# Optimization experiments

Measured on AMD Instinct MI355X. Metric: run time of the kernel, lower is better.

The kernel has to match this reference:

```python
import jax, jax.numpy as jnp
import numpy as np

NUM_HEADS = 8
TAU = 2.0
BN_EPS = 1e-5


def _make_atan_spike(alpha):
    @jax.custom_vjp
    def spike(x):
        return (x >= 0.0).astype(x.dtype)
    def fwd(x):
        return spike(x), x
    def bwd(x, g):
        sg = (alpha / 2.0) / (1.0 + (jnp.pi / 2.0 * alpha * x) ** 2)
        return (g * sg,)
    spike.defvjp(fwd, bwd)
    return spike


def _make_sigmoid_spike(alpha):
    @jax.custom_vjp
    def spike(x):
        return (x >= 0.0).astype(x.dtype)
    def fwd(x):
        return spike(x), x
    def bwd(x, g):
        s = jax.nn.sigmoid(alpha * x)
        return (g * alpha * s * (1.0 - s),)
    spike.defvjp(fwd, bwd)
    return spike

_atan_spike = _make_atan_spike(5.0)       # surrogate.ATan(alpha=5.0)
_sigmoid_spike = _make_sigmoid_spike(4.0)  # spikingjelly default surrogate.Sigmoid(alpha=4.0)


def lif_multistep(x_seq, v_threshold, spike_fn):
    """Multi-step LIF, tau=2, hard reset to 0, detach_reset=True, decay_input=True.
    x_seq: [T, ...]. Returns spike sequence [T, ...]."""
    def step(v, x):
        h = v + (x - v) / TAU
        s = spike_fn(h - v_threshold)
        sd = jax.lax.stop_gradient(s)  # detach_reset
        v_new = h * (1.0 - sd)         # hard reset to v_reset=0
        return v_new, s
    _, s_seq = jax.lax.scan(step, jnp.zeros_like(x_seq[0]), x_seq)
    return s_seq


def bn(x, gamma, beta, mean, var):
    # inference-mode BatchNorm1d over channel dim C of [T,B,C,N]
    inv = gamma / jnp.sqrt(var + BN_EPS)
    return (x - mean[None, None, :, None]) * inv[None, None, :, None] + beta[None, None, :, None]


def setup_inputs() -> dict:
    key = jax.random.key(0)
    T, B, C, H, W = 4, 32, 384, 16, 16
    ks = jax.random.split(key, 20)
    d = {"x": jax.random.normal(ks[0], (T, B, C, H, W), dtype=jnp.float32)}
    std = 1.0 / np.sqrt(C)
    for i, p in enumerate(["q", "k", "proj"]):
        d[p + "_w"] = jax.random.normal(ks[1 + 5 * i], (C, C), dtype=jnp.float32) * std
        d[p + "_gamma"] = jnp.ones((C,), jnp.float32) + 0.1 * jax.random.normal(ks[2 + 5 * i], (C,))
        d[p + "_beta"] = 0.1 * jax.random.normal(ks[3 + 5 * i], (C,))
        d[p + "_mean"] = 0.1 * jax.random.normal(ks[4 + 5 * i], (C,))
        d[p + "_var"] = jax.random.uniform(ks[5 + 5 * i], (C,), minval=0.5, maxval=1.5)
    d["proj_b"] = 0.01 * jax.random.normal(ks[16], (C,))
    return d


def reference(x, q_w, q_gamma, q_beta, q_mean, q_var,
              k_w, k_gamma, k_beta, k_mean, k_var,
              proj_w, proj_gamma, proj_beta, proj_mean, proj_var, proj_b):
    T, B, C, H, W = x.shape
    N = H * W
    Ch = C // NUM_HEADS
    xf = x.reshape(T, B, C, N)

    # q branch: 1x1 conv (C x C matmul) -> BN -> LIF
    q = bn(jnp.einsum('tbcn,dc->tbdn', xf, q_w), q_gamma, q_beta, q_mean, q_var)
    q = lif_multistep(q, 1.0, _atan_spike)
    q = q.reshape(T, B, NUM_HEADS, Ch, N)
    q = jnp.sum(q, axis=3, keepdims=True)          # [T,B,h,1,N]
    attn = lif_multistep(q, 0.5, _sigmoid_spike)    # attn_lif, v_threshold=0.5

    # k branch
    k = bn(jnp.einsum('tbcn,dc->tbdn', xf, k_w), k_gamma, k_beta, k_mean, k_var)
    k = lif_multistep(k, 1.0, _atan_spike)
    k = k.reshape(T, B, NUM_HEADS, Ch, N)

    y = (attn * k).reshape(T, B, C, N)

    # proj: 1x1 conv with bias -> BN -> LIF
    y = jnp.einsum('tbcn,dc->tbdn', y, proj_w) + proj_b[None, None, :, None]
    y = bn(y, proj_gamma, proj_beta, proj_mean, proj_var)
    y = lif_multistep(y, 1.0, _atan_spike)
    return y.reshape(T, B, C, H, W)
```

## Files before the change

kernel.cpp:

```cpp
#include <hip/hip_runtime.h>

typedef _Float16 f16x8 __attribute__((ext_vector_type(8)));
typedef _Float16 f16x4 __attribute__((ext_vector_type(4)));
typedef float    f32x4 __attribute__((ext_vector_type(4)));

#define TT 4
#define BB 32
#define CC 384
#define NN 256

#define WS_X1   25165824
#define WS_WSP  50331648
#define WS_Y    52101120
#define WS_NEED 77266944

__global__ __launch_bounds__(256) void wprep(
    const float* __restrict__ qw, const float* __restrict__ kw,
    const float* __restrict__ pw, _Float16* __restrict__ wsp)
{
    int gid   = blockIdx.x * 256 + threadIdx.x;
    int which = gid / 18432;
    int sid   = gid % 18432;
    int frag  = sid >> 6;
    int lane  = sid & 63;
    int h  = frag / 36;
    int rm = frag % 36;
    int dt = rm / 12, kc = rm % 12;
    int m16 = lane & 15, quad = lane >> 4;
    int d = h * 48 + dt * 16 + m16;

    const float* src = (which == 0) ? qw : (which == 1) ? kw : pw;
    _Float16* o0 = wsp + (size_t)which * 294912;
    _Float16* o1 = o0 + 147456;

    f16x8 h0, h1;
#pragma unroll
    for (int j = 0; j < 8; ++j) {
        int cp = kc * 32 + quad * 8 + j;
        int c;
        if (which == 2) {
            int hp = cp / 48, w = cp % 48;
            int qp = w / 12, r12 = w % 12;
            int sl = r12 >> 2, rr = r12 & 3;
            c = hp * 48 + sl * 16 + qp * 4 + rr;
        } else {
            c = cp;
        }
        float v = src[d * CC + c];
        _Float16 a = (_Float16)v;
        h0[j] = a; h1[j] = (_Float16)(v - (float)a);
    }
    size_t off = (size_t)frag * 512 + lane * 8;
    *(f16x8*)(o0 + off) = h0;
    *(f16x8*)(o1 + off) = h1;
}

__global__ __launch_bounds__(256) void xprep(
    const float* __restrict__ x, _Float16* __restrict__ x0,
    _Float16* __restrict__ x1)
{
    __shared__ float xs[64 * 65];
    const int tid = threadIdx.x;
    int bid = blockIdx.x;
    int tb = bid / 24, r = bid % 24;
    int c0 = (r >> 2) * 64, n0 = (r & 3) * 64;

#pragma unroll
    for (int p = 0; p < 4; ++p) {
        int c  = (tid >> 4) + p * 16;
        int nl = (tid & 15) * 4;
        float4 v = *(const float4*)&x[((size_t)tb * CC + c0 + c) * NN + n0 + nl];
        *(float4*)&xs[c * 65 + nl] = v;
    }
    __syncthreads();
#pragma unroll
    for (int p = 0; p < 2; ++p) {
        int sid  = p * 256 + tid;
        int frag = sid >> 6;
        int lane = sid & 63;
        int kcl  = frag & 1, n16l = frag >> 1;
        int m16 = lane & 15, quad = lane >> 4;
        int n_local = n16l * 16 + m16;
        int c_local = kcl * 32 + quad * 8;
        f16x8 h0, h1;
#pragma unroll
        for (int j = 0; j < 8; ++j) {
            float v = xs[(c_local + j) * 65 + n_local];
            _Float16 a = (_Float16)v;
            h0[j] = a; h1[j] = (_Float16)(v - (float)a);
        }
        size_t gf = ((size_t)tb * 16 + (n0 >> 4) + n16l) * 12 + (c0 >> 5) + kcl;
        size_t off = gf * 512 + lane * 8;
        *(f16x8*)(x0 + off) = h0;
        *(f16x8*)(x1 + off) = h1;
    }
}

__global__ __launch_bounds__(256, 3) void qk_mfma(
    const _Float16* __restrict__ x0, const _Float16* __restrict__ x1,
    const _Float16* __restrict__ wsp,
    const float* __restrict__ qg, const float* __restrict__ qbe,
    const float* __restrict__ qm, const float* __restrict__ qva,
    const float* __restrict__ kg, const float* __restrict__ kbe,
    const float* __restrict__ km, const float* __restrict__ kva,
    _Float16* __restrict__ y)
{
    const int tid  = threadIdx.x;
    const int wave = tid >> 6;
    const int lane = tid & 63;
    const int m16  = lane & 15;
    const int quad = lane >> 4;

    int bid = blockIdx.x;
    int r   = bid & 7;
    int hh  = (bid >> 3) & 1;
    int qq  = bid >> 4;
    int j   = qq * 8 + r;
    int b   = j >> 4;
    int n16 = j & 15;

    const int head = hh * 4 + wave;

    const _Float16* wq0 = wsp;
    const _Float16* wq1 = wsp + 147456;
    const _Float16* wk0 = wsp + 2 * 147456;
    const _Float16* wk1 = wsp + 3 * 147456;

    size_t fxb[4];
#pragma unroll
    for (int t = 0; t < 4; ++t)
        fxb[t] = (((size_t)(t * BB + b) * 16 + n16) * 12) * 512 + lane * 8;
    size_t fwb = ((size_t)head * 36) * 512 + lane * 8;

    f32x4 aq[4][3], ak[4][3];
#pragma unroll
    for (int t = 0; t < 4; ++t)
#pragma unroll
        for (int dt = 0; dt < 3; ++dt) {
            aq[t][dt] = (f32x4){0.f, 0.f, 0.f, 0.f};
            ak[t][dt] = (f32x4){0.f, 0.f, 0.f, 0.f};
        }

    for (int kc = 0; kc < 12; ++kc) {
        f16x8 bx[4][2];
#pragma unroll
        for (int t = 0; t < 4; ++t) {
            bx[t][0] = *(const f16x8*)(x0 + fxb[t] + kc * 512);
            bx[t][1] = *(const f16x8*)(x1 + fxb[t] + kc * 512);
        }
#pragma unroll
        for (int dt = 0; dt < 3; ++dt) {
            size_t wo = fwb + (size_t)(dt * 12 + kc) * 512;
            f16x8 q0 = *(const f16x8*)(wq0 + wo);
            f16x8 q1 = *(const f16x8*)(wq1 + wo);
            f16x8 k0 = *(const f16x8*)(wk0 + wo);
            f16x8 k1 = *(const f16x8*)(wk1 + wo);
#pragma unroll
            for (int t = 0; t < 4; ++t) {
                f32x4 cq = aq[t][dt];
                cq = __builtin_amdgcn_mfma_f32_16x16x32_f16(q0, bx[t][0], cq, 0, 0, 0);
                cq = __builtin_amdgcn_mfma_f32_16x16x32_f16(q1, bx[t][0], cq, 0, 0, 0);
                cq = __builtin_amdgcn_mfma_f32_16x16x32_f16(q0, bx[t][1], cq, 0, 0, 0);
                aq[t][dt] = cq;
                f32x4 ck = ak[t][dt];
                ck = __builtin_amdgcn_mfma_f32_16x16x32_f16(k0, bx[t][0], ck, 0, 0, 0);
                ck = __builtin_amdgcn_mfma_f32_16x16x32_f16(k1, bx[t][0], ck, 0, 0, 0);
                ck = __builtin_amdgcn_mfma_f32_16x16x32_f16(k0, bx[t][1], ck, 0, 0, 0);
                ak[t][dt] = ck;
            }
        }
    }

    f32x4 vq[3], vk[3];
    float va = 0.f;
#pragma unroll
    for (int dt = 0; dt < 3; ++dt) {
        vq[dt] = (f32x4){0.f, 0.f, 0.f, 0.f};
        vk[dt] = (f32x4){0.f, 0.f, 0.f, 0.f};
    }
#pragma unroll
    for (int t = 0; t < 4; ++t) {
        float psum = 0.f;
        f32x4 ks[3];
#pragma unroll
        for (int dt = 0; dt < 3; ++dt) {
            int doff = head * 48 + dt * 16 + quad * 4;
            f32x4 gq  = *(const f32x4*)(qg + doff);
            f32x4 bq  = *(const f32x4*)(qbe + doff);
            f32x4 mq  = *(const f32x4*)(qm + doff);
            f32x4 vq_ = *(const f32x4*)(qva + doff);
            f32x4 gk_ = *(const f32x4*)(kg + doff);
            f32x4 bk_ = *(const f32x4*)(kbe + doff);
            f32x4 mk_ = *(const f32x4*)(km + doff);
            f32x4 vk_ = *(const f32x4*)(kva + doff);
#pragma unroll
            for (int rr = 0; rr < 4; ++rr) {
                float invq = gq[rr] / sqrtf(vq_[rr] + 1e-5f);
                float invk = gk_[rr] / sqrtf(vk_[rr] + 1e-5f);
                float bnq = (aq[t][dt][rr] - mq[rr]) * invq + bq[rr];
                float hq  = vq[dt][rr] + (bnq - vq[dt][rr]) * 0.5f;
                float sq  = (hq - 1.0f >= 0.0f) ? 1.0f : 0.0f;
                vq[dt][rr] = hq * (1.0f - sq);
                psum += sq;
                float bnk = (ak[t][dt][rr] - mk_[rr]) * invk + bk_[rr];
                float hk  = vk[dt][rr] + (bnk - vk[dt][rr]) * 0.5f;
                float sk  = (hk - 1.0f >= 0.0f) ? 1.0f : 0.0f;
                vk[dt][rr] = hk * (1.0f - sk);
                ks[dt][rr] = sk;
            }
        }
        psum += __shfl_xor(psum, 16, 64);
        psum += __shfl_xor(psum, 32, 64);
        float ha = va + (psum - va) * 0.5f;
        float sa = (ha - 0.5f >= 0.0f) ? 1.0f : 0.0f;
        va = ha * (1.0f - sa);
        float attn = sa;
        size_t ybase = (((size_t)(t * BB + b) * 16 + n16) * 12) * 512;
#pragma unroll
        for (int dt = 0; dt < 3; ++dt) {
            int c   = head * 48 + quad * 12 + dt * 4;
            int kcy = c >> 5;
            int qp  = (c & 31) >> 3;
            int jj  = c & 7;
            f16x4 hv;
#pragma unroll
            for (int rr = 0; rr < 4; ++rr)
                hv[rr] = (_Float16)(attn * ks[dt][rr]);
            *(f16x4*)(y + ybase + (size_t)kcy * 512 + (m16 + 16 * qp) * 8 + jj) = hv;
        }
    }
}

__global__ __launch_bounds__(256, 4) void proj_mfma(
    const _Float16* __restrict__ y,
    const _Float16* __restrict__ pw0, const _Float16* __restrict__ pw1,
    const float* __restrict__ pg, const float* __restrict__ pbe,
    const float* __restrict__ pm, const float* __restrict__ pva,
    const float* __restrict__ pbias, float* __restrict__ out)
{
    const int tid  = threadIdx.x;
    const int wave = tid >> 6;
    const int lane = tid & 63;
    const int m16  = lane & 15;
    const int quad = lane >> 4;

    int bid = blockIdx.x;
    int r   = bid & 7;
    int dgg = (bid >> 3) & 1;
    int qq  = bid >> 4;
    int j   = qq * 8 + r;
    int b   = j >> 4;
    int n16 = j & 15;

    const int dw = dgg * 4 + wave;
    const int d0 = dw * 48;

    size_t fyb[4];
#pragma unroll
    for (int t = 0; t < 4; ++t)
        fyb[t] = (((size_t)(t * BB + b) * 16 + n16) * 12) * 512 + lane * 8;
    size_t fwb = ((size_t)dw * 36) * 512 + lane * 8;

    f32x4 acc[4][3];
#pragma unroll
    for (int t = 0; t < 4; ++t)
#pragma unroll
        for (int dt = 0; dt < 3; ++dt)
            acc[t][dt] = (f32x4){0.f, 0.f, 0.f, 0.f};

    for (int kc = 0; kc < 12; ++kc) {
        f16x8 by[4];
#pragma unroll
        for (int t = 0; t < 4; ++t)
            by[t] = *(const f16x8*)(y + fyb[t] + kc * 512);
#pragma unroll
        for (int dt = 0; dt < 3; ++dt) {
            size_t wo = fwb + (size_t)(dt * 12 + kc) * 512;
            f16x8 a0 = *(const f16x8*)(pw0 + wo);
            f16x8 a1 = *(const f16x8*)(pw1 + wo);
#pragma unroll
            for (int t = 0; t < 4; ++t) {
                f32x4 c = acc[t][dt];
                c = __builtin_amdgcn_mfma_f32_16x16x32_f16(a0, by[t], c, 0, 0, 0);
                c = __builtin_amdgcn_mfma_f32_16x16x32_f16(a1, by[t], c, 0, 0, 0);
                acc[t][dt] = c;
            }
        }
    }
    f32x4 vv[3];
#pragma unroll
    for (int dt = 0; dt < 3; ++dt) vv[dt] = (f32x4){0.f, 0.f, 0.f, 0.f};
#pragma unroll
    for (int dt = 0; dt < 3; ++dt) {
        int doff = d0 + dt * 16 + quad * 4;
        f32x4 g   = *(const f32x4*)(pg + doff);
        f32x4 be  = *(const f32x4*)(pbe + doff);
        f32x4 mu  = *(const f32x4*)(pm + doff);
        f32x4 va_ = *(const f32x4*)(pva + doff);
        f32x4 bi  = *(const f32x4*)(pbias + doff);
        float inv[4];
#pragma unroll
        for (int rr = 0; rr < 4; ++rr)
            inv[rr] = g[rr] / sqrtf(va_[rr] + 1e-5f);
#pragma unroll
        for (int t = 0; t < 4; ++t) {
#pragma unroll
            for (int rr = 0; rr < 4; ++rr) {
                float z  = acc[t][dt][rr] + bi[rr];
                float bn = (z - mu[rr]) * inv[rr] + be[rr];
                float h  = vv[dt][rr] + (bn - vv[dt][rr]) * 0.5f;
                float sp = (h - 1.0f >= 0.0f) ? 1.0f : 0.0f;
                vv[dt][rr] = h * (1.0f - sp);
                out[((size_t)(t * BB + b) * CC + doff + rr) * NN +
                    n16 * 16 + m16] = sp;
            }
        }
    }
}

#define KC 64
#define LSTR 68
__global__ __launch_bounds__(256) void qk_fused(
    const float* __restrict__ x,
    const float* __restrict__ qw, const float* __restrict__ qg,
    const float* __restrict__ qbe, const float* __restrict__ qm,
    const float* __restrict__ qva,
    const float* __restrict__ kw, const float* __restrict__ kg,
    const float* __restrict__ kbe, const float* __restrict__ km,
    const float* __restrict__ kva,
    unsigned char* __restrict__ y)
{
    __shared__ float xs[KC * LSTR];
    __shared__ float qws[48 * LSTR];
    __shared__ float kws[48 * LSTR];
    __shared__ float hsum[16 * 64];
    const int tid = threadIdx.x, bid = blockIdx.x;
    const int b = bid >> 5, head = (bid >> 2) & 7, n0 = (bid & 3) << 6;
    const int dg = tid >> 4, nl = (tid & 15) << 2;
    float q_inv[3], q_mu[3], q_b[3], k_inv[3], k_mu[3], k_b[3];
#pragma unroll
    for (int i = 0; i < 3; ++i) {
        int d = head * 48 + dg * 3 + i;
        q_inv[i] = qg[d] / sqrtf(qva[d] + 1e-5f); q_mu[i] = qm[d]; q_b[i] = qbe[d];
        k_inv[i] = kg[d] / sqrtf(kva[d] + 1e-5f); k_mu[i] = km[d]; k_b[i] = kbe[d];
    }
    float vq[3][4] = {}, vk[3][4] = {}, va[4] = {};
    for (int t = 0; t < TT; ++t) {
        float accq[3][4] = {}, acck[3][4] = {};
        for (int kc = 0; kc < CC / KC; ++kc) {
            const int c0 = kc * KC;
            __syncthreads();
#pragma unroll
            for (int p = 0; p < 4; ++p) {
                int q4 = tid + p * 256, cc = q4 >> 4, nn = (q4 & 15) << 2;
                *(float4*)&xs[cc * LSTR + nn] =
                    *(const float4*)&x[((size_t)(t * BB + b) * CC + c0 + cc) * NN + n0 + nn];
            }
#pragma unroll
            for (int p = 0; p < 3; ++p) {
                int q4 = tid + p * 256, dl = q4 >> 4, cc = (q4 & 15) << 2;
                *(float4*)&qws[dl * LSTR + cc] = *(const float4*)&qw[(head * 48 + dl) * CC + c0 + cc];
                *(float4*)&kws[dl * LSTR + cc] = *(const float4*)&kw[(head * 48 + dl) * CC + c0 + cc];
            }
            __syncthreads();
#pragma unroll
            for (int cq = 0; cq < KC / 4; ++cq) {
                float xv[4][4];
#pragma unroll
                for (int uu = 0; uu < 4; ++uu)
                    *(float4*)&xv[uu][0] = *(const float4*)&xs[(cq * 4 + uu) * LSTR + nl];
#pragma unroll
                for (int i = 0; i < 3; ++i) {
                    float qv[4], kv[4];
                    *(float4*)&qv[0] = *(const float4*)&qws[(dg * 3 + i) * LSTR + cq * 4];
                    *(float4*)&kv[0] = *(const float4*)&kws[(dg * 3 + i) * LSTR + cq * 4];
#pragma unroll
                    for (int uu = 0; uu < 4; ++uu)
#pragma unroll
                        for (int jj = 0; jj < 4; ++jj) {
                            accq[i][jj] = fmaf(qv[uu], xv[uu][jj], accq[i][jj]);
                            acck[i][jj] = fmaf(kv[uu], xv[uu][jj], acck[i][jj]);
                        }
                }
            }
        }
        float part[4] = {0.f, 0.f, 0.f, 0.f};
        float ksp[3][4];
#pragma unroll
        for (int i = 0; i < 3; ++i)
#pragma unroll
            for (int jj = 0; jj < 4; ++jj) {
                float bnq = (accq[i][jj] - q_mu[i]) * q_inv[i] + q_b[i];
                float hq = vq[i][jj] + (bnq - vq[i][jj]) * 0.5f;
                float sq = (hq - 1.0f >= 0.0f) ? 1.0f : 0.0f;
                vq[i][jj] = hq * (1.0f - sq); part[jj] += sq;
                float bnk = (acck[i][jj] - k_mu[i]) * k_inv[i] + k_b[i];
                float hk = vk[i][jj] + (bnk - vk[i][jj]) * 0.5f;
                float sk = (hk - 1.0f >= 0.0f) ? 1.0f : 0.0f;
                vk[i][jj] = hk * (1.0f - sk); ksp[i][jj] = sk;
            }
#pragma unroll
        for (int jj = 0; jj < 4; ++jj) hsum[dg * 64 + nl + jj] = part[jj];
        __syncthreads();
        float attn[4];
#pragma unroll
        for (int jj = 0; jj < 4; ++jj) {
            float tot = 0.f;
#pragma unroll
            for (int g = 0; g < 16; ++g) tot += hsum[g * 64 + nl + jj];
            float ha = va[jj] + (tot - va[jj]) * 0.5f;
            float sa = (ha - 0.5f >= 0.0f) ? 1.0f : 0.0f;
            va[jj] = ha * (1.0f - sa); attn[jj] = sa;
        }
#pragma unroll
        for (int i = 0; i < 3; ++i) {
            uchar4 yo;
            yo.x = (unsigned char)(attn[0] * ksp[i][0]);
            yo.y = (unsigned char)(attn[1] * ksp[i][1]);
            yo.z = (unsigned char)(attn[2] * ksp[i][2]);
            yo.w = (unsigned char)(attn[3] * ksp[i][3]);
            *(uchar4*)&((unsigned char*)y)[((size_t)(t * BB + b) * CC + head * 48 + dg * 3 + i) * NN + n0 + nl] = yo;
        }
    }
}

__global__ __launch_bounds__(256) void proj_fused(
    const unsigned char* __restrict__ yin,
    const float* __restrict__ pw, const float* __restrict__ pg,
    const float* __restrict__ pbe, const float* __restrict__ pm,
    const float* __restrict__ pva, const float* __restrict__ pbias,
    float* __restrict__ out)
{
    __shared__ float ys[KC * LSTR];
    __shared__ float pws[64 * LSTR];
    const int tid = threadIdx.x, bid = blockIdx.x;
    const int b = bid / 24, r = bid % 24, d0 = (r >> 2) * 64, n0 = (r & 3) << 6;
    const int dg = tid >> 4, nl = (tid & 15) << 2;
    float inv[4], mu[4], be[4], bi[4];
#pragma unroll
    for (int i = 0; i < 4; ++i) {
        int d = d0 + dg * 4 + i;
        inv[i] = pg[d] / sqrtf(pva[d] + 1e-5f);
        mu[i] = pm[d]; be[i] = pbe[d]; bi[i] = pbias[d];
    }
    float vvv[4][4] = {};
    for (int t = 0; t < TT; ++t) {
        float acc[4][4] = {};
        for (int kc = 0; kc < CC / KC; ++kc) {
            const int c0 = kc * KC;
            __syncthreads();
#pragma unroll
            for (int p = 0; p < 4; ++p) {
                int q4 = tid + p * 256, cc = q4 >> 4, nn = (q4 & 15) << 2;
                unsigned int w = *(const unsigned int*)&yin[((size_t)(t * BB + b) * CC + c0 + cc) * NN + n0 + nn];
                ys[cc * LSTR + nn + 0] = (float)(w & 0xff);
                ys[cc * LSTR + nn + 1] = (float)((w >> 8) & 0xff);
                ys[cc * LSTR + nn + 2] = (float)((w >> 16) & 0xff);
                ys[cc * LSTR + nn + 3] = (float)(w >> 24);
                *(float4*)&pws[cc * LSTR + nn] = *(const float4*)&pw[(d0 + cc) * CC + c0 + nn];
            }
            __syncthreads();
#pragma unroll
            for (int cq = 0; cq < KC / 4; ++cq) {
                float xv[4][4];
#pragma unroll
                for (int uu = 0; uu < 4; ++uu)
                    *(float4*)&xv[uu][0] = *(const float4*)&ys[(cq * 4 + uu) * LSTR + nl];
#pragma unroll
                for (int i = 0; i < 4; ++i) {
                    float pv[4];
                    *(float4*)&pv[0] = *(const float4*)&pws[(dg * 4 + i) * LSTR + cq * 4];
#pragma unroll
                    for (int uu = 0; uu < 4; ++uu)
#pragma unroll
                        for (int jj = 0; jj < 4; ++jj)
                            acc[i][jj] = fmaf(pv[uu], xv[uu][jj], acc[i][jj]);
                }
            }
        }
#pragma unroll
        for (int i = 0; i < 4; ++i) {
            float res[4];
#pragma unroll
            for (int jj = 0; jj < 4; ++jj) {
                float z = acc[i][jj] + bi[i];
                float bnv = (z - mu[i]) * inv[i] + be[i];
                float h = vvv[i][jj] + (bnv - vvv[i][jj]) * 0.5f;
                float sx = (h - 1.0f >= 0.0f) ? 1.0f : 0.0f;
                vvv[i][jj] = h * (1.0f - sx);
                res[jj] = sx;
            }
            *(float4*)&out[((size_t)(t * BB + b) * CC + d0 + dg * 4 + i) * NN + n0 + nl] = *(float4*)&res[0];
        }
    }
}

extern "C" void kernel_launch(void* const* d_in, const int* in_sizes, int n_in,
                              void* d_out, int out_size, void* d_ws, size_t ws_size,
                              hipStream_t stream)
{
    const float* x     = (const float*)d_in[0];
    const float* qw    = (const float*)d_in[1];
    const float* qg    = (const float*)d_in[2];
    const float* qbe   = (const float*)d_in[3];
    const float* qm    = (const float*)d_in[4];
    const float* qva   = (const float*)d_in[5];
    const float* kw    = (const float*)d_in[6];
    const float* kg    = (const float*)d_in[7];
    const float* kbe   = (const float*)d_in[8];
    const float* km    = (const float*)d_in[9];
    const float* kva   = (const float*)d_in[10];
    const float* pw    = (const float*)d_in[11];
    const float* pg    = (const float*)d_in[12];
    const float* pbe   = (const float*)d_in[13];
    const float* pm    = (const float*)d_in[14];
    const float* pva   = (const float*)d_in[15];
    const float* pbias = (const float*)d_in[16];
    float* out = (float*)d_out;

    if (ws_size >= (size_t)WS_NEED) {
        char* w = (char*)d_ws;
        _Float16* x0  = (_Float16*)(w);
        _Float16* x1  = (_Float16*)(w + WS_X1);
        _Float16* wsp = (_Float16*)(w + WS_WSP);
        _Float16* pw0 = wsp + 4 * 147456;
        _Float16* pw1 = wsp + 5 * 147456;
        _Float16* yf  = (_Float16*)(w + WS_Y);

        wprep<<<216, 256, 0, stream>>>(qw, kw, pw, wsp);
        xprep<<<3072, 256, 0, stream>>>(x, x0, x1);
        qk_mfma<<<1024, 256, 0, stream>>>(x0, x1, wsp, qg, qbe, qm, qva,
                                          kg, kbe, km, kva, yf);
        proj_mfma<<<1024, 256, 0, stream>>>(yf, pw0, pw1, pg, pbe, pm, pva,
                                            pbias, out);
    } else {
        unsigned char* y = (unsigned char*)d_ws;
        qk_fused<<<BB * 8 * (NN / 64), 256, 0, stream>>>(
            x, qw, qg, qbe, qm, qva, kw, kg, kbe, km, kva, y);
        proj_fused<<<BB * (CC / 64) * (NN / 64), 256, 0, stream>>>(
            y, pw, pg, pbe, pm, pva, pbias, out);
    }
}
```

Measured before the change: 246.2 us.

## Merge prep kernels and double-buffer activation loads in MFMA GEMM loops

```diff
diff --git a/kernel.cpp b/kernel.cpp
--- a/kernel.cpp
+++ b/kernel.cpp
@@ -14,54 +14,56 @@
 #define WS_Y    52101120
 #define WS_NEED 77266944
 
-__global__ __launch_bounds__(256) void wprep(
+__global__ __launch_bounds__(256) void prep(
+    const float* __restrict__ x,
     const float* __restrict__ qw, const float* __restrict__ kw,
-    const float* __restrict__ pw, _Float16* __restrict__ wsp)
-{
-    int gid   = blockIdx.x * 256 + threadIdx.x;
-    int which = gid / 18432;
-    int sid   = gid % 18432;
-    int frag  = sid >> 6;
-    int lane  = sid & 63;
-    int h  = frag / 36;
-    int rm = frag % 36;
-    int dt = rm / 12, kc = rm % 12;
-    int m16 = lane & 15, quad = lane >> 4;
-    int d = h * 48 + dt * 16 + m16;
-
-    const float* src = (which == 0) ? qw : (which == 1) ? kw : pw;
-    _Float16* o0 = wsp + (size_t)which * 294912;
-    _Float16* o1 = o0 + 147456;
-
-    f16x8 h0, h1;
-#pragma unroll
-    for (int j = 0; j < 8; ++j) {
-        int cp = kc * 32 + quad * 8 + j;
-        int c;
-        if (which == 2) {
-            int hp = cp / 48, w = cp % 48;
-            int qp = w / 12, r12 = w % 12;
-            int sl = r12 >> 2, rr = r12 & 3;
-            c = hp * 48 + sl * 16 + qp * 4 + rr;
-        } else {
-            c = cp;
-        }
-        float v = src[d * CC + c];
-        _Float16 a = (_Float16)v;
-        h0[j] = a; h1[j] = (_Float16)(v - (float)a);
-    }
-    size_t off = (size_t)frag * 512 + lane * 8;
-    *(f16x8*)(o0 + off) = h0;
-    *(f16x8*)(o1 + off) = h1;
-}
-
-__global__ __launch_bounds__(256) void xprep(
-    const float* __restrict__ x, _Float16* __restrict__ x0,
-    _Float16* __restrict__ x1)
+    const float* __restrict__ pw,
+    _Float16* __restrict__ x0, _Float16* __restrict__ x1,
+    _Float16* __restrict__ wsp)
 {
     __shared__ float xs[64 * 65];
     const int tid = threadIdx.x;
     int bid = blockIdx.x;
+
+    if (bid >= 3072) {
+        int gid   = (bid - 3072) * 256 + tid;
+        int which = gid / 18432;
+        int sid   = gid % 18432;
+        int frag  = sid >> 6;
+        int lane  = sid & 63;
+        int h  = frag / 36;
+        int rm = frag % 36;
+        int dt = rm / 12, kc = rm % 12;
+        int m16 = lane & 15, quad = lane >> 4;
+        int d = h * 48 + dt * 16 + m16;
+
+        const float* src = (which == 0) ? qw : (which == 1) ? kw : pw;
+        _Float16* o0 = wsp + (size_t)which * 294912;
+        _Float16* o1 = o0 + 147456;
+
+        f16x8 h0, h1;
+#pragma unroll
+        for (int jj = 0; jj < 8; ++jj) {
+            int cp = kc * 32 + quad * 8 + jj;
+            int c;
+            if (which == 2) {
+                int hp = cp / 48, w = cp % 48;
+                int qp = w / 12, r12 = w % 12;
+                int sl = r12 >> 2, rr = r12 & 3;
+                c = hp * 48 + sl * 16 + qp * 4 + rr;
+            } else {
+                c = cp;
+            }
+            float v = src[d * CC + c];
+            _Float16 a = (_Float16)v;
+            h0[jj] = a; h1[jj] = (_Float16)(v - (float)a);
+        }
+        size_t off = (size_t)frag * 512 + lane * 8;
+        *(f16x8*)(o0 + off) = h0;
+        *(f16x8*)(o1 + off) = h1;
+        return;
+    }
+
     int tb = bid / 24, r = bid % 24;
     int c0 = (r >> 2) * 64, n0 = (r & 3) * 64;
 
@@ -84,10 +86,10 @@
         int c_local = kcl * 32 + quad * 8;
         f16x8 h0, h1;
 #pragma unroll
-        for (int j = 0; j < 8; ++j) {
-            float v = xs[(c_local + j) * 65 + n_local];
+        for (int jj = 0; jj < 8; ++jj) {
+            float v = xs[(c_local + jj) * 65 + n_local];
             _Float16 a = (_Float16)v;
-            h0[j] = a; h1[j] = (_Float16)(v - (float)a);
+            h0[jj] = a; h1[jj] = (_Float16)(v - (float)a);
         }
         size_t gf = ((size_t)tb * 16 + (n0 >> 4) + n16l) * 12 + (c0 >> 5) + kcl;
         size_t off = gf * 512 + lane * 8;
@@ -96,7 +98,43 @@
     }
 }
 
-__global__ __launch_bounds__(256, 3) void qk_mfma(
+#define QK_LOADX(dst, kcv)                                                   \
+    {                                                                        \
+        _Pragma("unroll")                                                    \
+        for (int t = 0; t < 4; ++t) {                                        \
+            dst[t][0] = *(const f16x8*)(pxb0[t] + (kcv) * 512 + lo);         \
+            dst[t][1] = *(const f16x8*)(pxb1[t] + (kcv) * 512 + lo);         \
+        }                                                                    \
+    }
+
+#define QK_STEP(kcv, bxv)                                                    \
+    {                                                                        \
+        f16x8 w[4][3];                                                       \
+        _Pragma("unroll")                                                    \
+        for (int brs = 0; brs < 4; ++brs)                                    \
+            _Pragma("unroll")                                                \
+            for (int dt = 0; dt < 3; ++dt)                                   \
+                w[brs][dt] = *(const f16x8*)(wt[brs] +                       \
+                    (dt * 12 + (kcv)) * 512 + lo);                           \
+        _Pragma("unroll")                                                    \
+        for (int dt = 0; dt < 3; ++dt) {                                     \
+            _Pragma("unroll")                                                \
+            for (int t = 0; t < 4; ++t) {                                    \
+                f32x4 cq = aq[t][dt];                                        \
+                cq = __builtin_amdgcn_mfma_f32_16x16x32_f16(w[0][dt], bxv[t][0], cq, 0, 0, 0); \
+                cq = __builtin_amdgcn_mfma_f32_16x16x32_f16(w[1][dt], bxv[t][0], cq, 0, 0, 0); \
+                cq = __builtin_amdgcn_mfma_f32_16x16x32_f16(w[0][dt], bxv[t][1], cq, 0, 0, 0); \
+                aq[t][dt] = cq;                                              \
+                f32x4 ck = ak[t][dt];                                        \
+                ck = __builtin_amdgcn_mfma_f32_16x16x32_f16(w[2][dt], bxv[t][0], ck, 0, 0, 0); \
+                ck = __builtin_amdgcn_mfma_f32_16x16x32_f16(w[3][dt], bxv[t][0], ck, 0, 0, 0); \
+                ck = __builtin_amdgcn_mfma_f32_16x16x32_f16(w[2][dt], bxv[t][1], ck, 0, 0, 0); \
+                ak[t][dt] = ck;                                              \
+            }                                                                \
+        }                                                                    \
+    }
+
+__global__ __launch_bounds__(256, 2) void qk_mfma(
     const _Float16* __restrict__ x0, const _Float16* __restrict__ x1,
     const _Float16* __restrict__ wsp,
     const float* __restrict__ qg, const float* __restrict__ qbe,
@@ -110,6 +148,7 @@
     const int lane = tid & 63;
     const int m16  = lane & 15;
     const int quad = lane >> 4;
+    const int lo   = lane * 8;
 
     int bid = blockIdx.x;
     int r   = bid & 7;
@@ -121,16 +160,18 @@
 
     const int head = hh * 4 + wave;
 
-    const _Float16* wq0 = wsp;
-    const _Float16* wq1 = wsp + 147456;
-    const _Float16* wk0 = wsp + 2 * 147456;
-    const _Float16* wk1 = wsp + 3 * 147456;
-
-    size_t fxb[4];
-#pragma unroll
-    for (int t = 0; t < 4; ++t)
-        fxb[t] = (((size_t)(t * BB + b) * 16 + n16) * 12) * 512 + lane * 8;
-    size_t fwb = ((size_t)head * 36) * 512 + lane * 8;
+    const _Float16* pxb0[4];
+    const _Float16* pxb1[4];
+#pragma unroll
+    for (int t = 0; t < 4; ++t) {
+        size_t off = (((size_t)(t * BB + b) * 16 + n16) * 12) * 512;
+        pxb0[t] = x0 + off;
+        pxb1[t] = x1 + off;
+    }
+    const _Float16* wt[4];
+#pragma unroll
+    for (int brs = 0; brs < 4; ++brs)
+        wt[brs] = wsp + (size_t)brs * 147456 + (size_t)head * 36 * 512;
 
     f32x4 aq[4][3], ak[4][3];
 #pragma unroll
@@ -141,33 +182,34 @@
             ak[t][dt] = (f32x4){0.f, 0.f, 0.f, 0.f};
         }
 
-    for (int kc = 0; kc < 12; ++kc) {
-        f16x8 bx[4][2];
-#pragma unroll
-        for (int t = 0; t < 4; ++t) {
-            bx[t][0] = *(const f16x8*)(x0 + fxb[t] + kc * 512);
-            bx[t][1] = *(const f16x8*)(x1 + fxb[t] + kc * 512);
-        }
-#pragma unroll
-        for (int dt = 0; dt < 3; ++dt) {
-            size_t wo = fwb + (size_t)(dt * 12 + kc) * 512;
-            f16x8 q0 = *(const f16x8*)(wq0 + wo);
-            f16x8 q1 = *(const f16x8*)(wq1 + wo);
-            f16x8 k0 = *(const f16x8*)(wk0 + wo);
-            f16x8 k1 = *(const f16x8*)(wk1 + wo);
-#pragma unroll
-            for (int t = 0; t < 4; ++t) {
-                f32x4 cq = aq[t][dt];
-                cq = __builtin_amdgcn_mfma_f32_16x16x32_f16(q0, bx[t][0], cq, 0, 0, 0);
-                cq = __builtin_amdgcn_mfma_f32_16x16x32_f16(q1, bx[t][0], cq, 0, 0, 0);
-                cq = __builtin_amdgcn_mfma_f32_16x16x32_f16(q0, bx[t][1], cq, 0, 0, 0);
-                aq[t][dt] = cq;
-                f32x4 ck = ak[t][dt];
-                ck = __builtin_amdgcn_mfma_f32_16x16x32_f16(k0, bx[t][0], ck, 0, 0, 0);
-                ck = __builtin_amdgcn_mfma_f32_16x16x32_f16(k1, bx[t][0], ck, 0, 0, 0);
-                ck = __builtin_amdgcn_mfma_f32_16x16x32_f16(k0, bx[t][1], ck, 0, 0, 0);
-                ak[t][dt] = ck;
-            }
+    f16x8 bxA[4][2], bxB[4][2];
+    QK_LOADX(bxA, 0)
+#pragma unroll
+    for (int kc2 = 0; kc2 < 6; ++kc2) {
+        QK_LOADX(bxB, 2 * kc2 + 1)
+        QK_STEP(2 * kc2, bxA)
+        if (kc2 < 5)
+            QK_LOADX(bxA, 2 * kc2 + 2)
+        QK_STEP(2 * kc2 + 1, bxB)
+    }
+
+    float invq[3][4], invk[3][4];
+    f32x4 mqv[3], bqv[3], mkv[3], bkv[3];
+#pragma unroll
+    for (int dt = 0; dt < 3; ++dt) {
+        int doff = head * 48 + dt * 16 + quad * 4;
+        f32x4 gq  = *(const f32x4*)(qg + doff);
+        f32x4 vq_ = *(const f32x4*)(qva + doff);
+        f32x4 gk_ = *(const f32x4*)(kg + doff);
+        f32x4 vk_ = *(const f32x4*)(kva + doff);
+        mqv[dt] = *(const f32x4*)(qm + doff);
+        bqv[dt] = *(const f32x4*)(qbe + doff);
+        mkv[dt] = *(const f32x4*)(km + doff);
+        bkv[dt] = *(const f32x4*)(kbe + doff);
+#pragma unroll
+        for (int rr = 0; rr < 4; ++rr) {
+            invq[dt][rr] = gq[rr] / sqrtf(vq_[rr] + 1e-5f);
+            invk[dt][rr] = gk_[rr] / sqrtf(vk_[rr] + 1e-5f);
         }
     }
 
@@ -184,25 +226,14 @@
         f32x4 ks[3];
 #pragma unroll
         for (int dt = 0; dt < 3; ++dt) {
-            int doff = head * 48 + dt * 16 + quad * 4;
-            f32x4 gq  = *(const f32x4*)(qg + doff);
-            f32x4 bq  = *(const f32x4*)(qbe + doff);
-            f32x4 mq  = *(const f32x4*)(qm + doff);
-            f32x4 vq_ = *(const f32x4*)(qva + doff);
-            f32x4 gk_ = *(const f32x4*)(kg + doff);
-            f32x4 bk_ = *(const f32x4*)(kbe + doff);
-            f32x4 mk_ = *(const f32x4*)(km + doff);
-            f32x4 vk_ = *(const f32x4*)(kva + doff);
 #pragma unroll
             for (int rr = 0; rr < 4; ++rr) {
-                float invq = gq[rr] / sqrtf(vq_[rr] + 1e-5f);
-                float invk = gk_[rr] / sqrtf(vk_[rr] + 1e-5f);
-                float bnq = (aq[t][dt][rr] - mq[rr]) * invq + bq[rr];
+                float bnq = (aq[t][dt][rr] - mqv[dt][rr]) * invq[dt][rr] + bqv[dt][rr];
                 float hq  = vq[dt][rr] + (bnq - vq[dt][rr]) * 0.5f;
                 float sq  = (hq - 1.0f >= 0.0f) ? 1.0f : 0.0f;
                 vq[dt][rr] = hq * (1.0f - sq);
                 psum += sq;
-                float bnk = (ak[t][dt][rr] - mk_[rr]) * invk + bk_[rr];
+                float bnk = (ak[t][dt][rr] - mkv[dt][rr]) * invk[dt][rr] + bkv[dt][rr];
                 float hk  = vk[dt][rr] + (bnk - vk[dt][rr]) * 0.5f;
                 float sk  = (hk - 1.0f >= 0.0f) ? 1.0f : 0.0f;
                 vk[dt][rr] = hk * (1.0f - sk);
@@ -231,7 +262,35 @@
     }
 }
 
-__global__ __launch_bounds__(256, 4) void proj_mfma(
+#define PJ_LOADY(dst, kcv)                                                   \
+    {                                                                        \
+        _Pragma("unroll")                                                    \
+        for (int t = 0; t < 4; ++t)                                          \
+            dst[t] = *(const f16x8*)(pyb[t] + (kcv) * 512 + lo);             \
+    }
+
+#define PJ_STEP(kcv, byv)                                                    \
+    {                                                                        \
+        f16x8 w[2][3];                                                       \
+        _Pragma("unroll")                                                    \
+        for (int sp = 0; sp < 2; ++sp)                                       \
+            _Pragma("unroll")                                                \
+            for (int dt = 0; dt < 3; ++dt)                                   \
+                w[sp][dt] = *(const f16x8*)(pwt[sp] +                        \
+                    (dt * 12 + (kcv)) * 512 + lo);                           \
+        _Pragma("unroll")                                                    \
+        for (int dt = 0; dt < 3; ++dt) {                                     \
+            _Pragma("unroll")                                                \
+            for (int t = 0; t < 4; ++t) {                                    \
+                f32x4 c = acc[t][dt];                                        \
+                c = __builtin_amdgcn_mfma_f32_16x16x32_f16(w[0][dt], byv[t], c, 0, 0, 0); \
+                c = __builtin_amdgcn_mfma_f32_16x16x32_f16(w[1][dt], byv[t], c, 0, 0, 0); \
+                acc[t][dt] = c;                                              \
+            }                                                                \
+        }                                                                    \
+    }
+
+__global__ __launch_bounds__(256, 2) void proj_mfma(
     const _Float16* __restrict__ y,
     const _Float16* __restrict__ pw0, const _Float16* __restrict__ pw1,
     const float* __restrict__ pg, const float* __restrict__ pbe,
@@ -243,6 +302,7 @@
     const int lane = tid & 63;
     const int m16  = lane & 15;
     const int quad = lane >> 4;
+    const int lo   = lane * 8;
 
     int bid = blockIdx.x;
     int r   = bid & 7;
@@ -255,11 +315,13 @@
     const int dw = dgg * 4 + wave;
     const int d0 = dw * 48;
 
-    size_t fyb[4];
+    const _Float16* pyb[4];
 #pragma unroll
     for (int t = 0; t < 4; ++t)
-        fyb[t] = (((size_t)(t * BB + b) * 16 + n16) * 12) * 512 + lane * 8;
-    size_t fwb = ((size_t)dw * 36) * 512 + lane * 8;
+        pyb[t] = y + (((size_t)(t * BB + b) * 16 + n16) * 12) * 512;
+    const _Float16* pwt[2];
+    pwt[0] = pw0 + (size_t)dw * 36 * 512;
+    pwt[1] = pw1 + (size_t)dw * 36 * 512;
 
     f32x4 acc[4][3];
 #pragma unroll
@@ -268,32 +330,24 @@
         for (int dt = 0; dt < 3; ++dt)
             acc[t][dt] = (f32x4){0.f, 0.f, 0.f, 0.f};
 
-    for (int kc = 0; kc < 12; ++kc) {
-        f16x8 by[4];
-#pragma unroll
-        for (int t = 0; t < 4; ++t)
-            by[t] = *(const f16x8*)(y + fyb[t] + kc * 512);
-#pragma unroll
-        for (int dt = 0; dt < 3; ++dt) {
-            size_t wo = fwb + (size_t)(dt * 12 + kc) * 512;
-            f16x8 a0 = *(const f16x8*)(pw0 + wo);
-            f16x8 a1 = *(const f16x8*)(pw1 + wo);
-#pragma unroll
-            for (int t = 0; t < 4; ++t) {
-                f32x4 c = acc[t][dt];
-                c = __builtin_amdgcn_mfma_f32_16x16x32_f16(a0, by[t], c, 0, 0, 0);
-                c = __builtin_amdgcn_mfma_f32_16x16x32_f16(a1, by[t], c, 0, 0, 0);
-                acc[t][dt] = c;
-            }
-        }
-    }
+    f16x8 byA[4], byB[4];
+    PJ_LOADY(byA, 0)
+#pragma unroll
+    for (int kc2 = 0; kc2 < 6; ++kc2) {
+        PJ_LOADY(byB, 2 * kc2 + 1)
+        PJ_STEP(2 * kc2, byA)
+        if (kc2 < 5)
+            PJ_LOADY(byA, 2 * kc2 + 2)
+        PJ_STEP(2 * kc2 + 1, byB)
+    }
+
     f32x4 vv[3];
 #pragma unroll
     for (int dt = 0; dt < 3; ++dt) vv[dt] = (f32x4){0.f, 0.f, 0.f, 0.f};
 #pragma unroll
     for (int dt = 0; dt < 3; ++dt) {
         int doff = d0 + dt * 16 + quad * 4;
-        f32x4 g   = *(const f32x4*)(pg + doff);
+        f32x4 g_  = *(const f32x4*)(pg + doff);
         f32x4 be  = *(const f32x4*)(pbe + doff);
         f32x4 mu  = *(const f32x4*)(pm + doff);
         f32x4 va_ = *(const f32x4*)(pva + doff);
@@ -301,7 +355,7 @@
         float inv[4];
 #pragma unroll
         for (int rr = 0; rr < 4; ++rr)
-            inv[rr] = g[rr] / sqrtf(va_[rr] + 1e-5f);
+            inv[rr] = g_[rr] / sqrtf(va_[rr] + 1e-5f);
 #pragma unroll
         for (int t = 0; t < 4; ++t) {
 #pragma unroll
@@ -527,8 +581,7 @@
         _Float16* pw1 = wsp + 5 * 147456;
         _Float16* yf  = (_Float16*)(w + WS_Y);
 
-        wprep<<<216, 256, 0, stream>>>(qw, kw, pw, wsp);
-        xprep<<<3072, 256, 0, stream>>>(x, x0, x1);
+        prep<<<3288, 256, 0, stream>>>(x, qw, kw, pw, x0, x1, wsp);
         qk_mfma<<<1024, 256, 0, stream>>>(x0, x1, wsp, qg, qbe, qm, qva,
                                           kg, kbe, km, kva, yf);
         proj_mfma<<<1024, 256, 0, stream>>>(yf, pw0, pw1, pg, pbe, pm, pva,
```

Result: faster. 222.2 us (-9.7%).
